# Optimization experiments

Measured on AMD Instinct MI355X. Metric: run time of the kernel, lower is better.

## Reference

```python
import jax, jax.numpy as jnp
import numpy as np

N_NODES = 100000
N_EDGES = 1600000
IN_DIM = 128
OUT_DIM = 64


def setup_inputs() -> dict:
    key = jax.random.key(0)
    k1, k2, k3, k4, k5, k6 = jax.random.split(key, 6)
    x = jax.random.normal(k1, (N_NODES, IN_DIM), dtype=jnp.float32)
    edge_row = jax.random.randint(k2, (N_EDGES,), 0, N_NODES, dtype=jnp.int32)
    edge_col = jax.random.randint(k3, (N_EDGES,), 0, N_NODES, dtype=jnp.int32)
    edge_val = jax.random.uniform(k4, (N_EDGES,), dtype=jnp.float32)
    W = jax.random.normal(k5, (IN_DIM, OUT_DIM), dtype=jnp.float32) * (1.0 / np.sqrt(IN_DIM))
    b = jax.random.normal(k6, (OUT_DIM,), dtype=jnp.float32) * 0.01
    return {"x": x, "edge_row": edge_row, "edge_col": edge_col,
            "edge_val": edge_val, "W": W, "b": b}


def reference(x, edge_row, edge_col, edge_val, W, b):
    # xw = Linear(x)  -> [N, OUT_DIM]
    xw = x @ W + b
    # SpMM: (A_hat @ xw)[r] = sum_e val[e] * xw[col[e]] for edges with row[e]==r
    msgs = edge_val[:, None] * xw[edge_col]          # [E, OUT_DIM]
    ax = jax.ops.segment_sum(msgs, edge_row, num_segments=N_NODES)  # [N, OUT_DIM]
    # ReLU; dropout p=0.0 is identity (eval mode)
    return jax.nn.relu(ax)
```

## Files before the change

kernel.cpp:

```cpp
#include <hip/hip_runtime.h>
#include <hip/hip_fp16.h>
#include <limits.h>

#define IN_DIM 128
#define OUT_DIM 64
#define NBUCK 782
#define RPB 128
#define CHUNK 4096
#define SCAP 4096


typedef _Float16 half8_t __attribute__((ext_vector_type(8)));
typedef float    f32x4  __attribute__((ext_vector_type(4)));

__device__ __forceinline__ int kmap(int g, int j) {
    return g * 4 + (j & 3) + 16 * (j >> 2);
}

__global__ __launch_bounds__(256) void prep_kernel(
    const float* __restrict__ W, __half* __restrict__ wf,
    int* __restrict__ bcount, int* __restrict__ cursor) {
    const int t = threadIdx.x;
    for (int idx = t; idx < 4 * 4 * 64 * 8; idx += 256) {
        const int j    = idx & 7;
        const int lane = (idx >> 3) & 63;
        const int ks   = (idx >> 9) & 3;
        const int n    = idx >> 11;
        const int col  = n * 16 + (lane & 15);
        const int k    = ks * 32 + kmap(lane >> 4, j);
        wf[idx] = __float2half(W[k * OUT_DIM + col]);
    }
    if (bcount)
        for (int i = t; i < NBUCK; i += 256) { bcount[i] = 0; cursor[i] = 0; }
}

__global__ __launch_bounds__(256) void gemm_hist_kernel(
    const float* __restrict__ x, const __half* __restrict__ wf,
    const float* __restrict__ b, __half* __restrict__ xw, int n_nodes,
    const int* __restrict__ erow, int* __restrict__ bcount, int n_edges) {
    __shared__ int h[NBUCK];
    const int t  = threadIdx.x;
    const int l  = t & 63;
    const int wv = t >> 6;
    const int g  = l >> 4;
    const int rowbase = blockIdx.x * 64 + wv * 16;
    const int row = rowbase + (l & 15);
    const bool rok = row < n_nodes;
    const float* xr = x + (size_t)row * IN_DIM;

    half8_t bf[4][4];
    const half8_t* wf8 = (const half8_t*)wf;
    #pragma unroll
    for (int n = 0; n < 4; ++n)
        #pragma unroll
        for (int ks = 0; ks < 4; ++ks)
            bf[n][ks] = wf8[(n * 4 + ks) * 64 + l];

    half8_t af[4];
    #pragma unroll
    for (int ks = 0; ks < 4; ++ks) {
        float4 c0 = rok ? *(const float4*)(xr + ks * 32 + g * 4)
                        : make_float4(0.f, 0.f, 0.f, 0.f);
        float4 c1 = rok ? *(const float4*)(xr + ks * 32 + 16 + g * 4)
                        : make_float4(0.f, 0.f, 0.f, 0.f);
        half8_t a;
        a[0] = (_Float16)c0.x; a[1] = (_Float16)c0.y;
        a[2] = (_Float16)c0.z; a[3] = (_Float16)c0.w;
        a[4] = (_Float16)c1.x; a[5] = (_Float16)c1.y;
        a[6] = (_Float16)c1.z; a[7] = (_Float16)c1.w;
        af[ks] = a;
    }

    f32x4 acc[4];
    #pragma unroll
    for (int n = 0; n < 4; ++n) acc[n] = (f32x4){0.f, 0.f, 0.f, 0.f};

    #pragma unroll
    for (int ks = 0; ks < 4; ++ks)
        #pragma unroll
        for (int n = 0; n < 4; ++n)
            acc[n] = __builtin_amdgcn_mfma_f32_16x16x32_f16(af[ks], bf[n][ks], acc[n], 0, 0, 0);

    float bias[4];
    #pragma unroll
    for (int n = 0; n < 4; ++n) bias[n] = b[n * 16 + (l & 15)];

    #pragma unroll
    for (int n = 0; n < 4; ++n)
        #pragma unroll
        for (int q = 0; q < 4; ++q) {
            const int ro = rowbase + g * 4 + q;
            if (ro < n_nodes)
                xw[(size_t)ro * OUT_DIM + n * 16 + (l & 15)] =
                    __float2half(acc[n][q] + bias[n]);
        }

    if (bcount && blockIdx.x < 512) {
        for (int i = t; i < NBUCK; i += 256) h[i] = 0;
        __syncthreads();
        const int stride = 512 * 256;
        for (int e = blockIdx.x * 256 + t; e < n_edges; e += stride)
            atomicAdd(&h[erow[e] >> 7], 1);
        __syncthreads();
        for (int i = t; i < NBUCK; i += 256)
            if (h[i]) atomicAdd(&bcount[i], h[i]);
    }
}

__global__ __launch_bounds__(512) void partition_kernel(
    const int* __restrict__ erow, const int* __restrict__ ecol,
    const float* __restrict__ eval_, const int* __restrict__ bcount,
    int* __restrict__ cursor, int2* __restrict__ ecs, int n_edges) {
    __shared__ int  hist[NBUCK];
    __shared__ int  lbase[NBUCK];
    __shared__ int  gdelta[NBUCK];
    __shared__ int  sbase[NBUCK];
    __shared__ int2 data[CHUNK];
    __shared__ int  gpos[CHUNK];
    __shared__ int  wsum[8];

    const int t = threadIdx.x;
    const int base = blockIdx.x * CHUNK;
    const int cnt = min(CHUNK, n_edges - base);

    for (int i = t; i < NBUCK; i += 512) hist[i] = 0;

    {
        const int i0 = 2 * t, i1 = 2 * t + 1;
        const int v0 = (i0 < NBUCK) ? bcount[i0] : 0;
        const int v1 = (i1 < NBUCK) ? bcount[i1] : 0;
        const int s2 = v0 + v1;
        int inc = s2;
        #pragma unroll
        for (int d = 1; d < 64; d <<= 1) {
            int u = __shfl_up(inc, d, 64);
            if ((t & 63) >= d) inc += u;
        }
        if ((t & 63) == 63) wsum[t >> 6] = inc;
        __syncthreads();
        int wp = 0;
        #pragma unroll
        for (int w = 0; w < 8; ++w) if (w < (t >> 6)) wp += wsum[w];
        const int ex = wp + (inc - s2);
        if (i0 < NBUCK) sbase[i0] = ex;
        if (i1 < NBUCK) sbase[i1] = ex + v0;
    }

    int   myrow[CHUNK / 512];
    int   mycol[CHUNK / 512];
    float myval[CHUNK / 512];
    #pragma unroll
    for (int i = 0; i < CHUNK / 512; ++i) {
        const int idx = t + i * 512;
        if (idx < cnt) {
            const int e = base + idx;
            myrow[i] = erow[e];
            mycol[i] = ecol[e];
            myval[i] = eval_[e];
            atomicAdd(&hist[myrow[i] >> 7], 1);
        }
    }
    __syncthreads();

    {
        const int i0 = 2 * t, i1 = 2 * t + 1;
        const int v0 = (i0 < NBUCK) ? hist[i0] : 0;
        const int v1 = (i1 < NBUCK) ? hist[i1] : 0;
        const int s2 = v0 + v1;
        int inc = s2;
        #pragma unroll
        for (int d = 1; d < 64; d <<= 1) {
            int u = __shfl_up(inc, d, 64);
            if ((t & 63) >= d) inc += u;
        }
        if ((t & 63) == 63) wsum[t >> 6] = inc;
        __syncthreads();
        int wp = 0;
        #pragma unroll
        for (int w = 0; w < 8; ++w) if (w < (t >> 6)) wp += wsum[w];
        const int ex = wp + (inc - s2);
        if (i0 < NBUCK) lbase[i0] = ex;
        if (i1 < NBUCK) lbase[i1] = ex + v0;
    }
    __syncthreads();

    for (int i = t; i < NBUCK; i += 512) {
        const int c = hist[i];
        gdelta[i] = c ? (sbase[i] + atomicAdd(&cursor[i], c) - lbase[i]) : 0;
    }
    __syncthreads();

    #pragma unroll
    for (int i = 0; i < CHUNK / 512; ++i) {
        const int idx = t + i * 512;
        if (idx < cnt) {
            const int bk = myrow[i] >> 7;
            const int slot = atomicAdd(&lbase[bk], 1);
            int2 p;
            p.x = (int)(((unsigned)(myrow[i] & (RPB - 1)) << 25) |
                        ((unsigned)mycol[i] << 7));
            p.y = __float_as_int(myval[i]);
            data[slot] = p;
            gpos[slot] = slot + gdelta[bk];
        }
    }
    __syncthreads();

    for (int slot = t; slot < cnt; slot += 512)
        ecs[gpos[slot]] = data[slot];
}

__global__ __launch_bounds__(512) void bucket_gather_kernel(
    const __half* __restrict__ xw, const int2* __restrict__ ecs,
    const int* __restrict__ bcount, float* __restrict__ out,
    int n_nodes, int n_edges) {
    __shared__ int2 data[SCAP];
    __shared__ int  hist[RPB];
    __shared__ int  rstart[RPB + 1];
    __shared__ int  sbase[NBUCK + 1];
    __shared__ int  wsum[8];
    __shared__ int  wtot;

    const int bk   = blockIdx.x;
    const int t    = threadIdx.x;
    const int lane = t & 63;
    const int wv   = t >> 6;
    const int q    = lane & 7;
    const int g    = lane >> 3;

    if (t < RPB) hist[t] = 0;

    {
        const int i0 = 2 * t, i1 = 2 * t + 1;
        const int v0 = (i0 < NBUCK) ? bcount[i0] : 0;
        const int v1 = (i1 < NBUCK) ? bcount[i1] : 0;
        const int s2 = v0 + v1;
        int inc = s2;
        #pragma unroll
        for (int d = 1; d < 64; d <<= 1) {
            int u = __shfl_up(inc, d, 64);
            if ((t & 63) >= d) inc += u;
        }
        if ((t & 63) == 63) wsum[t >> 6] = inc;
        __syncthreads();
        int wp = 0;
        #pragma unroll
        for (int w = 0; w < 8; ++w) if (w < (t >> 6)) wp += wsum[w];
        const int ex = wp + (inc - s2);
        if (i0 < NBUCK) sbase[i0] = ex;
        if (i1 < NBUCK) sbase[i1] = ex + v0;
        if (t == 511) sbase[NBUCK] = wp + inc;
    }
    __syncthreads();

    const int s     = sbase[bk];
    const int e     = sbase[bk + 1];
    const int cnt   = e - s;
    const int rbase = bk * RPB;
    const char* xwb = (const char*)xw;

    if (cnt <= SCAP) {
        for (int i = t; i < cnt; i += 512)
            atomicAdd(&hist[((unsigned)ecs[s + i].x) >> 25], 1);
        __syncthreads();

        {
            int inc = 0, v = 0;
            if (t < RPB) {
                v = hist[t];
                inc = v;
                #pragma unroll
                for (int d = 1; d < 64; d <<= 1) {
                    int u = __shfl_up(inc, d, 64);
                    if ((t & 63) >= d) inc += u;
                }
                if (t == 63) wtot = inc;
            }
            __syncthreads();
            if (t < RPB) {
                if (t >= 64) inc += wtot;
                rstart[t] = inc - v;
                hist[t]   = inc - v;
                if (t == RPB - 1) rstart[RPB] = inc;
            }
        }
        __syncthreads();

        for (int i = t; i < cnt; i += 512) {
            const int2 p = ecs[s + i];
            const int pos = atomicAdd(&hist[((unsigned)p.x) >> 25], 1);
            data[pos] = p;
        }
        __syncthreads();

        for (int rp = 0; rp < 8; ++rp) {
            const int rl0 = wv * 16 + rp * 2;
            const int rl1 = rl0 + 1;
            int j0 = rstart[rl0];
            const int e0 = rstart[rl0 + 1];
            int j1 = rstart[rl1];
            const int e1 = rstart[rl1 + 1];

            float acc0[8], acc1[8];
            #pragma unroll
            for (int i = 0; i < 8; ++i) { acc0[i] = 0.f; acc1[i] = 0.f; }

            while (j0 < e0 || j1 < e1) {
                const bool a0 = j0 < e0;
                const bool a1 = j1 < e1;
                float v0 = 0.f, v1 = 0.f;
                unsigned off0 = 0, off1 = 0;
                if (a0) {
                    const int ei = j0 + g;
                    const int2 p = data[min(ei, cnt - 1)];
                    v0 = (ei < e0) ? __int_as_float(p.y) : 0.f;
                    off0 = (((unsigned)p.x) & 0x01FFFF80u) | ((unsigned)q << 4);
                }
                if (a1) {
                    const int ei = j1 + g;
                    const int2 p = data[min(ei, cnt - 1)];
                    v1 = (ei < e1) ? __int_as_float(p.y) : 0.f;
                    off1 = (((unsigned)p.x) & 0x01FFFF80u) | ((unsigned)q << 4);
                }
                union { uint4 u; __half2 h[4]; } U0, U1;
                if (a0) U0.u = *(const uint4*)(xwb + off0);
                if (a1) U1.u = *(const uint4*)(xwb + off1);
                if (a0) {
                    #pragma unroll
                    for (int i = 0; i < 4; ++i) {
                        const float2 f = __half22float2(U0.h[i]);
                        acc0[2 * i]     = fmaf(v0, f.x, acc0[2 * i]);
                        acc0[2 * i + 1] = fmaf(v0, f.y, acc0[2 * i + 1]);
                    }
                    j0 += 8;
                }
                if (a1) {
                    #pragma unroll
                    for (int i = 0; i < 4; ++i) {
                        const float2 f = __half22float2(U1.h[i]);
                        acc1[2 * i]     = fmaf(v1, f.x, acc1[2 * i]);
                        acc1[2 * i + 1] = fmaf(v1, f.y, acc1[2 * i + 1]);
                    }
                    j1 += 8;
                }
            }

            #pragma unroll
            for (int d = 8; d < 64; d <<= 1) {
                #pragma unroll
                for (int i = 0; i < 8; ++i) {
                    acc0[i] += __shfl_xor(acc0[i], d, 64);
                    acc1[i] += __shfl_xor(acc1[i], d, 64);
                }
            }

            if (g == 0) {
                const int r0 = rbase + rl0;
                const int r1 = rbase + rl1;
                if (r0 < n_nodes) {
                    float4 o0, o1;
                    o0.x = fmaxf(acc0[0], 0.f); o0.y = fmaxf(acc0[1], 0.f);
                    o0.z = fmaxf(acc0[2], 0.f); o0.w = fmaxf(acc0[3], 0.f);
                    o1.x = fmaxf(acc0[4], 0.f); o1.y = fmaxf(acc0[5], 0.f);
                    o1.z = fmaxf(acc0[6], 0.f); o1.w = fmaxf(acc0[7], 0.f);
                    float* op = out + (size_t)r0 * OUT_DIM + q * 8;
                    *(float4*)(op)     = o0;
                    *(float4*)(op + 4) = o1;
                }
                if (r1 < n_nodes) {
                    float4 o0, o1;
                    o0.x = fmaxf(acc1[0], 0.f); o0.y = fmaxf(acc1[1], 0.f);
                    o0.z = fmaxf(acc1[2], 0.f); o0.w = fmaxf(acc1[3], 0.f);
                    o1.x = fmaxf(acc1[4], 0.f); o1.y = fmaxf(acc1[5], 0.f);
                    o1.z = fmaxf(acc1[6], 0.f); o1.w = fmaxf(acc1[7], 0.f);
                    float* op = out + (size_t)r1 * OUT_DIM + q * 8;
                    *(float4*)(op)     = o0;
                    *(float4*)(op + 4) = o1;
                }
            }
        }
    } else {
        for (int rr = 0; rr < 16; ++rr) {
            const int r = rbase + wv * 16 + rr;
            if (r >= n_nodes) break;
            float acc[8];
            #pragma unroll
            for (int i = 0; i < 8; ++i) acc[i] = 0.f;
            const unsigned rl = (unsigned)(r & (RPB - 1));
            for (int j = s + g; j < e; j += 8) {
                const int2 p = ecs[j];
                if ((((unsigned)p.x) >> 25) == rl) {
                    const float v = __int_as_float(p.y);
                    const unsigned off = (((unsigned)p.x) & 0x01FFFF80u) | ((unsigned)q << 4);
                    union { uint4 u; __half2 h[4]; } U;
                    U.u = *(const uint4*)(xwb + off);
                    #pragma unroll
                    for (int i = 0; i < 4; ++i) {
                        const float2 f = __half22float2(U.h[i]);
                        acc[2 * i]     = fmaf(v, f.x, acc[2 * i]);
                        acc[2 * i + 1] = fmaf(v, f.y, acc[2 * i + 1]);
                    }
                }
            }
            #pragma unroll
            for (int d = 8; d < 64; d <<= 1)
                #pragma unroll
                for (int i = 0; i < 8; ++i)
                    acc[i] += __shfl_xor(acc[i], d, 64);
            if (g == 0) {
                float4 o0, o1;
                o0.x = fmaxf(acc[0], 0.f); o0.y = fmaxf(acc[1], 0.f);
                o0.z = fmaxf(acc[2], 0.f); o0.w = fmaxf(acc[3], 0.f);
                o1.x = fmaxf(acc[4], 0.f); o1.y = fmaxf(acc[5], 0.f);
                o1.z = fmaxf(acc[6], 0.f); o1.w = fmaxf(acc[7], 0.f);
                float* op = out + (size_t)r * OUT_DIM + q * 8;
                *(float4*)(op)     = o0;
                *(float4*)(op + 4) = o1;
            }
        }
    }
}

__global__ __launch_bounds__(256) void edge_scatter_kernel(
    const __half* __restrict__ xw, const int* __restrict__ erow,
    const int* __restrict__ ecol, const float* __restrict__ eval_,
    float* __restrict__ out, int n_edges) {
    const int lane  = threadIdx.x & 63;
    const int wid   = (blockIdx.x * blockDim.x + threadIdx.x) >> 6;
    const int nwave = (gridDim.x * blockDim.x) >> 6;
    for (int e = wid; e < n_edges; e += nwave) {
        const float m = eval_[e] * __half2float(xw[(size_t)ecol[e] * OUT_DIM + lane]);
        atomicAdd(&out[(size_t)erow[e] * OUT_DIM + lane], m);
    }
}

__global__ __launch_bounds__(256) void relu_kernel(float4* __restrict__ p, int n4) {
    const int stride = gridDim.x * blockDim.x;
    for (int i = blockIdx.x * blockDim.x + threadIdx.x; i < n4; i += stride) {
        float4 v = p[i];
        v.x = fmaxf(v.x, 0.f); v.y = fmaxf(v.y, 0.f);
        v.z = fmaxf(v.z, 0.f); v.w = fmaxf(v.w, 0.f);
        p[i] = v;
    }
}

extern "C" void kernel_launch(void* const* d_in, const int* in_sizes, int n_in,
                              void* d_out, int out_size, void* d_ws, size_t ws_size,
                              hipStream_t stream) {
    const float* x     = (const float*)d_in[0];
    const int*   erow  = (const int*)d_in[1];
    const int*   ecol  = (const int*)d_in[2];
    const float* eval_ = (const float*)d_in[3];
    const float* W     = (const float*)d_in[4];
    const float* b     = (const float*)d_in[5];
    float*       out   = (float*)d_out;

    const int n_nodes = in_sizes[0] / IN_DIM;
    const int n_edges = in_sizes[1];

    auto align256 = [](size_t v) { return (v + 255) & ~(size_t)255; };
    size_t off_xw     = 0;
    size_t off_wf     = align256(off_xw     + (size_t)n_nodes * OUT_DIM * 2);
    size_t off_bcount = align256(off_wf     + (size_t)4 * 4 * 64 * 8 * 2);
    size_t off_cursor = align256(off_bcount + (size_t)NBUCK * 4);
    size_t off_ecs    = align256(off_cursor + (size_t)NBUCK * 4);
    size_t need       = off_ecs + (size_t)n_edges * 8;

    __half* xw = (__half*)((char*)d_ws + off_xw);
    __half* wf = (__half*)((char*)d_ws + off_wf);

    const bool main_path = (need <= ws_size) && (n_nodes <= NBUCK * RPB) && (n_edges > 0);

    if (main_path) {
        int*  bcount = (int*)((char*)d_ws + off_bcount);
        int*  cursor = (int*)((char*)d_ws + off_cursor);
        int2* ecs    = (int2*)((char*)d_ws + off_ecs);

        prep_kernel<<<1, 256, 0, stream>>>(W, wf, bcount, cursor);
        gemm_hist_kernel<<<(n_nodes + 63) / 64, 256, 0, stream>>>(
            x, wf, b, xw, n_nodes, erow, bcount, n_edges);
        partition_kernel<<<(n_edges + CHUNK - 1) / CHUNK, 512, 0, stream>>>(
            erow, ecol, eval_, bcount, cursor, ecs, n_edges);
        bucket_gather_kernel<<<NBUCK, 512, 0, stream>>>(
            xw, ecs, bcount, out, n_nodes, n_edges);
    } else {
        prep_kernel<<<1, 256, 0, stream>>>(W, wf, nullptr, nullptr);
        gemm_hist_kernel<<<(n_nodes + 63) / 64, 256, 0, stream>>>(
            x, wf, b, xw, n_nodes, nullptr, nullptr, 0);
        hipMemsetAsync(d_out, 0, (size_t)out_size * sizeof(float), stream);
        edge_scatter_kernel<<<8192, 256, 0, stream>>>(xw, erow, ecol, eval_, out, n_edges);
        relu_kernel<<<2048, 256, 0, stream>>>((float4*)d_out, out_size / 4);
    }
}
```

Before: 106.1 us.

## Split each gather bucket across two blocks and precompute bucket offsets in partition

The gather kernel now launches two blocks per 128-row bucket, each handling 64 rows. That doubles the grid and halves shared-memory staging per block, which should raise occupancy. Bucket start offsets are computed once by the partition kernel and written to a global array, so the gather blocks no longer redo the prefix scan over all bucket counts. In exchange, each block reads the whole bucket's edge list twice (once to count rows, once to fill its own half) and filters by row half, which doubles global reads of the packed edges.

```diff
diff --git a/kernel.cpp b/kernel.cpp
--- a/kernel.cpp
+++ b/kernel.cpp
@@ -6,8 +6,9 @@
 #define OUT_DIM 64
 #define NBUCK 782
 #define RPB 128
+#define HRPB 64
 #define CHUNK 4096
-#define SCAP 4096
+#define SCAP2 2048
 
 
 typedef _Float16 half8_t __attribute__((ext_vector_type(8)));
@@ -110,7 +111,8 @@
 __global__ __launch_bounds__(512) void partition_kernel(
     const int* __restrict__ erow, const int* __restrict__ ecol,
     const float* __restrict__ eval_, const int* __restrict__ bcount,
-    int* __restrict__ cursor, int2* __restrict__ ecs, int n_edges) {
+    int* __restrict__ cursor, int2* __restrict__ ecs,
+    int* __restrict__ bbase, int n_edges) {
     __shared__ int  hist[NBUCK];
     __shared__ int  lbase[NBUCK];
     __shared__ int  gdelta[NBUCK];
@@ -144,6 +146,12 @@
         const int ex = wp + (inc - s2);
         if (i0 < NBUCK) sbase[i0] = ex;
         if (i1 < NBUCK) sbase[i1] = ex + v0;
+    }
+    __syncthreads();
+
+    if (blockIdx.x == 0) {
+        for (int i = t; i < NBUCK; i += 512) bbase[i] = sbase[i];
+        if (t == 0) bbase[NBUCK] = n_edges;
     }
 
     int   myrow[CHUNK / 512];
@@ -212,89 +220,65 @@
 
 __global__ __launch_bounds__(512) void bucket_gather_kernel(
     const __half* __restrict__ xw, const int2* __restrict__ ecs,
-    const int* __restrict__ bcount, float* __restrict__ out,
+    const int* __restrict__ bbase, float* __restrict__ out,
     int n_nodes, int n_edges) {
-    __shared__ int2 data[SCAP];
-    __shared__ int  hist[RPB];
-    __shared__ int  rstart[RPB + 1];
-    __shared__ int  sbase[NBUCK + 1];
-    __shared__ int  wsum[8];
-    __shared__ int  wtot;
-
-    const int bk   = blockIdx.x;
+    __shared__ int2 data[SCAP2];
+    __shared__ int  hist[HRPB];
+    __shared__ int  rstart[HRPB + 1];
+
+    const int bk2  = blockIdx.x;
+    const int bk   = bk2 >> 1;
+    const int half = bk2 & 1;
     const int t    = threadIdx.x;
     const int lane = t & 63;
     const int wv   = t >> 6;
     const int q    = lane & 7;
     const int g    = lane >> 3;
 
-    if (t < RPB) hist[t] = 0;
-
-    {
-        const int i0 = 2 * t, i1 = 2 * t + 1;
-        const int v0 = (i0 < NBUCK) ? bcount[i0] : 0;
-        const int v1 = (i1 < NBUCK) ? bcount[i1] : 0;
-        const int s2 = v0 + v1;
-        int inc = s2;
+    const int s   = bbase[bk];
+    const int e   = bbase[bk + 1];
+    const int cnt = e - s;
+    const int rowbase = bk * RPB + half * HRPB;
+    const char* xwb = (const char*)xw;
+
+    if (t < HRPB) hist[t] = 0;
+    __syncthreads();
+
+    for (int i = t; i < cnt; i += 512) {
+        const unsigned rl = ((unsigned)ecs[s + i].x) >> 25;
+        if ((int)(rl >> 6) == half) atomicAdd(&hist[rl & (HRPB - 1)], 1);
+    }
+    __syncthreads();
+
+    if (t < HRPB) {
+        const int v = hist[t];
+        int inc = v;
         #pragma unroll
         for (int d = 1; d < 64; d <<= 1) {
             int u = __shfl_up(inc, d, 64);
-            if ((t & 63) >= d) inc += u;
-        }
-        if ((t & 63) == 63) wsum[t >> 6] = inc;
-        __syncthreads();
-        int wp = 0;
-        #pragma unroll
-        for (int w = 0; w < 8; ++w) if (w < (t >> 6)) wp += wsum[w];
-        const int ex = wp + (inc - s2);
-        if (i0 < NBUCK) sbase[i0] = ex;
-        if (i1 < NBUCK) sbase[i1] = ex + v0;
-        if (t == 511) sbase[NBUCK] = wp + inc;
-    }
-    __syncthreads();
-
-    const int s     = sbase[bk];
-    const int e     = sbase[bk + 1];
-    const int cnt   = e - s;
-    const int rbase = bk * RPB;
-    const char* xwb = (const char*)xw;
-
-    if (cnt <= SCAP) {
-        for (int i = t; i < cnt; i += 512)
-            atomicAdd(&hist[((unsigned)ecs[s + i].x) >> 25], 1);
-        __syncthreads();
-
-        {
-            int inc = 0, v = 0;
-            if (t < RPB) {
-                v = hist[t];
-                inc = v;
-                #pragma unroll
-                for (int d = 1; d < 64; d <<= 1) {
-                    int u = __shfl_up(inc, d, 64);
-                    if ((t & 63) >= d) inc += u;
-                }
-                if (t == 63) wtot = inc;
-            }
-            __syncthreads();
-            if (t < RPB) {
-                if (t >= 64) inc += wtot;
-                rstart[t] = inc - v;
-                hist[t]   = inc - v;
-                if (t == RPB - 1) rstart[RPB] = inc;
-            }
-        }
-        __syncthreads();
-
+            if (t >= d) inc += u;
+        }
+        rstart[t] = inc - v;
+        hist[t]   = inc - v;
+        if (t == HRPB - 1) rstart[HRPB] = inc;
+    }
+    __syncthreads();
+
+    const int cntH = rstart[HRPB];
+
+    if (cntH <= SCAP2) {
         for (int i = t; i < cnt; i += 512) {
             const int2 p = ecs[s + i];
-            const int pos = atomicAdd(&hist[((unsigned)p.x) >> 25], 1);
-            data[pos] = p;
+            const unsigned rl = ((unsigned)p.x) >> 25;
+            if ((int)(rl >> 6) == half) {
+                const int pos = atomicAdd(&hist[rl & (HRPB - 1)], 1);
+                data[pos] = p;
+            }
         }
         __syncthreads();
 
-        for (int rp = 0; rp < 8; ++rp) {
-            const int rl0 = wv * 16 + rp * 2;
+        for (int rp = 0; rp < 4; ++rp) {
+            const int rl0 = wv * 8 + rp * 2;
             const int rl1 = rl0 + 1;
             int j0 = rstart[rl0];
             const int e0 = rstart[rl0 + 1];
@@ -312,13 +296,13 @@
                 unsigned off0 = 0, off1 = 0;
                 if (a0) {
                     const int ei = j0 + g;
-                    const int2 p = data[min(ei, cnt - 1)];
+                    const int2 p = data[min(ei, cntH - 1)];
                     v0 = (ei < e0) ? __int_as_float(p.y) : 0.f;
                     off0 = (((unsigned)p.x) & 0x01FFFF80u) | ((unsigned)q << 4);
                 }
                 if (a1) {
                     const int ei = j1 + g;
-                    const int2 p = data[min(ei, cnt - 1)];
+                    const int2 p = data[min(ei, cntH - 1)];
                     v1 = (ei < e1) ? __int_as_float(p.y) : 0.f;
                     off1 = (((unsigned)p.x) & 0x01FFFF80u) | ((unsigned)q << 4);
                 }
@@ -355,8 +339,8 @@
             }
 
             if (g == 0) {
-                const int r0 = rbase + rl0;
-                const int r1 = rbase + rl1;
+                const int r0 = rowbase + rl0;
+                const int r1 = rowbase + rl1;
                 if (r0 < n_nodes) {
                     float4 o0, o1;
                     o0.x = fmaxf(acc0[0], 0.f); o0.y = fmaxf(acc0[1], 0.f);
@@ -380,8 +364,8 @@
             }
         }
     } else {
-        for (int rr = 0; rr < 16; ++rr) {
-            const int r = rbase + wv * 16 + rr;
+        for (int rr = 0; rr < 8; ++rr) {
+            const int r = rowbase + wv * 8 + rr;
             if (r >= n_nodes) break;
             float acc[8];
             #pragma unroll
@@ -463,7 +447,8 @@
     size_t off_wf     = align256(off_xw     + (size_t)n_nodes * OUT_DIM * 2);
     size_t off_bcount = align256(off_wf     + (size_t)4 * 4 * 64 * 8 * 2);
     size_t off_cursor = align256(off_bcount + (size_t)NBUCK * 4);
-    size_t off_ecs    = align256(off_cursor + (size_t)NBUCK * 4);
+    size_t off_bbase  = align256(off_cursor + (size_t)NBUCK * 4);
+    size_t off_ecs    = align256(off_bbase  + (size_t)(NBUCK + 1) * 4);
     size_t need       = off_ecs + (size_t)n_edges * 8;
 
     __half* xw = (__half*)((char*)d_ws + off_xw);
@@ -474,15 +459,16 @@
     if (main_path) {
         int*  bcount = (int*)((char*)d_ws + off_bcount);
         int*  cursor = (int*)((char*)d_ws + off_cursor);
+        int*  bbase  = (int*)((char*)d_ws + off_bbase);
         int2* ecs    = (int2*)((char*)d_ws + off_ecs);
 
         prep_kernel<<<1, 256, 0, stream>>>(W, wf, bcount, cursor);
         gemm_hist_kernel<<<(n_nodes + 63) / 64, 256, 0, stream>>>(
             x, wf, b, xw, n_nodes, erow, bcount, n_edges);
         partition_kernel<<<(n_edges + CHUNK - 1) / CHUNK, 512, 0, stream>>>(
-            erow, ecol, eval_, bcount, cursor, ecs, n_edges);
-        bucket_gather_kernel<<<NBUCK, 512, 0, stream>>>(
-            xw, ecs, bcount, out, n_nodes, n_edges);
+            erow, ecol, eval_, bcount, cursor, ecs, bbase, n_edges);
+        bucket_gather_kernel<<<NBUCK * 2, 512, 0, stream>>>(
+            xw, ecs, bbase, out, n_nodes, n_edges);
     } else {
         prep_kernel<<<1, 256, 0, stream>>>(W, wf, nullptr, nullptr);
         gemm_hist_kernel<<<(n_nodes + 63) / 64, 256, 0, stream>>>(
```

Result: no change. 105.0 us (-1.0%).
